# Performance work log

Measured on AMD Instinct MI355X. Metric: run time of the kernel, lower is better.

The kernel has to match this reference:

```python
import jax, jax.numpy as jnp
import numpy as np

HIDDEN = 1024
MOE_INTER = 512
SHARED_INTER = 2048
N_EXPERTS = 32
TOP_K = 6
N_GROUP = 8
TOPK_GROUP = 4
ROUTED_SCALE = 2.5


def setup_inputs() -> dict:
    key = jax.random.key(0)
    ks = jax.random.split(key, 6)
    s = 0.02
    return {
        "hidden_states": jax.random.normal(ks[0], (2, 1024, HIDDEN), jnp.float32),
        "gate_w": jax.random.normal(ks[1], (N_EXPERTS, HIDDEN), jnp.float32) * s,
        "e_bias": jnp.zeros((N_EXPERTS,), jnp.float32),  # e_score_correction_bias (non-trainable)
        "up_w": jax.random.normal(ks[2], (N_EXPERTS, MOE_INTER, HIDDEN), jnp.float32) * s,
        "down_w": jax.random.normal(ks[3], (N_EXPERTS, HIDDEN, MOE_INTER), jnp.float32) * s,
        "shared_up_w": jax.random.normal(ks[4], (SHARED_INTER, HIDDEN), jnp.float32) * s,
        "shared_down_w": jax.random.normal(ks[5], (HIDDEN, SHARED_INTER), jnp.float32) * s,
    }


def _relu2(x):
    # Nemotron-H 'relu2' activation: relu(x)^2
    return jnp.square(jax.nn.relu(x))


def _router(x, gate_w, e_bias):
    # x: [T, H] -> topk_idx [T, K] (int), topk_w [T, K] (fp32)
    T = x.shape[0]
    logits = x.astype(jnp.float32) @ gate_w.astype(jnp.float32).T  # [T, E]
    scores = jax.nn.sigmoid(logits)
    sc = scores + e_bias[None, :]
    # group-limited routing: top-2 sum per group, keep topk_group groups
    g = sc.reshape(T, N_GROUP, N_EXPERTS // N_GROUP)
    group_scores = jax.lax.top_k(g, 2)[0].sum(-1)                  # [T, G]
    group_idx = jax.lax.top_k(group_scores, TOPK_GROUP)[1]         # [T, TG]
    group_mask = jnp.zeros_like(group_scores).at[jnp.arange(T)[:, None], group_idx].set(1.0)
    score_mask = jnp.repeat(group_mask, N_EXPERTS // N_GROUP, axis=1)  # [T, E]
    masked = jnp.where(score_mask > 0, sc, 0.0)
    topk_idx = jax.lax.stop_gradient(jax.lax.top_k(masked, TOP_K)[1])  # torch path is @no_grad
    topk_w = jnp.take_along_axis(scores, topk_idx, axis=1)         # gather from unbiased scores
    topk_w = topk_w / (topk_w.sum(-1, keepdims=True) + 1e-20)      # norm_topk_prob
    topk_w = topk_w * ROUTED_SCALE
    return topk_idx, topk_w


def reference(hidden_states, gate_w, e_bias, up_w, down_w, shared_up_w, shared_down_w):
    B, S, H = hidden_states.shape
    x = hidden_states.reshape(-1, H)  # [T, H]
    T = x.shape[0]
    topk_idx, topk_w = _router(x, gate_w, e_bias)
    # combine weights as dense [T, E] (scatter of top-k weights)
    combine = jnp.zeros((T, N_EXPERTS), topk_w.dtype).at[jnp.arange(T)[:, None], topk_idx].add(topk_w)
    # dense-masked expert compute; weight applied on intermediate (equivalent since
    # down_proj is linear with no bias): out = sum_e w_te * down_e(act(up_e(x)))
    h = _relu2(jnp.einsum('th,eih->tei', x, up_w))   # [T, E, I]
    h = h * combine[:, :, None]
    moe_out = jnp.einsum('tei,ehi->th', h, down_w)   # [T, H]
    shared = _relu2(x @ shared_up_w.T) @ shared_down_w.T
    return (moe_out + shared).reshape(B, S, H)


if __name__ == "__main__":
    out = reference(**setup_inputs())
    print(out.shape, out.dtype)
```

## Files before the change

kernel.cpp:

```cpp
#include <hip/hip_runtime.h>

typedef unsigned short u16;
typedef __bf16 bf16x8 __attribute__((ext_vector_type(8)));
typedef float f32x4 __attribute__((ext_vector_type(4)));
typedef u16 u16x8 __attribute__((ext_vector_type(8)));

#define T_TOK 2048
#define HID   1024
#define NEXP  32
#define IM    512
#define SI    2048
#define TOPK  6
#define PLAN_MAX 160

__device__ __forceinline__ u16 f2bf(float f){
  unsigned u = __float_as_uint(f);
  u += 0x7FFFu + ((u >> 16) & 1u);
  return (u16)(u >> 16);
}

__device__ __forceinline__ void gll16(const void* g, void* l){
  __builtin_amdgcn_global_load_lds((const __attribute__((address_space(1))) void*)g,
                                   (__attribute__((address_space(3))) void*)l, 16, 0, 0);
}

__device__ __forceinline__ u16x8 cvt2(float4 a, float4 b){
  u16x8 o;
  o[0] = f2bf(a.x); o[1] = f2bf(a.y); o[2] = f2bf(a.z); o[3] = f2bf(a.w);
  o[4] = f2bf(b.x); o[5] = f2bf(b.y); o[6] = f2bf(b.z); o[7] = f2bf(b.w);
  return o;
}

__global__ __launch_bounds__(256) void prep_kernel(
    const float* __restrict__ x, const float4* __restrict__ upw, const float4* __restrict__ dnw,
    const float4* __restrict__ supw, const float4* __restrict__ sdnw,
    const float* __restrict__ gate, const float* __restrict__ ebias,
    u16x8* __restrict__ xb, u16x8* __restrict__ upb, u16x8* __restrict__ dnb,
    u16x8* __restrict__ supb, u16x8* __restrict__ sdnb,
    int* __restrict__ ce, float* __restrict__ cw, int* __restrict__ done){
  int blk = blockIdx.x;
  if (blk == 0 && threadIdx.x == 0) *done = 0;
  if (blk >= 512){
    const float4* s; u16x8* d; long i;
    if (blk < 16896){
      i = (long)(blk - 512) * 256 + threadIdx.x;
      if (i < 2097152L){ s = upw; d = upb; }
      else             { s = dnw; d = dnb; i -= 2097152L; }
    } else {
      i = (long)(blk - 16896) * 256 + threadIdx.x;
      if      (i < 262144L){ s = (const float4*)x; d = xb; }
      else if (i < 524288L){ s = supw; d = supb; i -= 262144L; }
      else                 { s = sdnw; d = sdnb; i -= 524288L; }
    }
    float4 a = s[2*i], b = s[2*i+1];
    d[i] = cvt2(a, b);
    return;
  }
  int wave = threadIdx.x >> 6;
  int lane = threadIdx.x & 63;
  int t = blk * 4 + wave;
  int e = lane & 31, half = lane >> 5;
  const float4* xv = (const float4*)(x + (size_t)t * HID);
  const float4* gv = (const float4*)(gate + (size_t)e * HID);
  double d0a = 0, d1a = 0, d2a = 0, d3a = 0;
  for (int i = half * 128; i < half * 128 + 128; i++){
    float4 a = xv[i], b = gv[i];
    d0a += (double)a.x * b.x; d1a += (double)a.y * b.y;
    d2a += (double)a.z * b.z; d3a += (double)a.w * b.w;
  }
  double acc = (d0a + d1a) + (d2a + d3a);
  acc += __shfl_xor(acc, 32);
  double score = 1.0 / (1.0 + exp(-acc));
  double sc = score + (double)ebias[e];
  double o1  = __shfl_xor(sc, 1);
  double hi  = fmax(sc, o1), lo = fmin(sc, o1);
  double ohi = __shfl_xor(hi, 2), olo = __shfl_xor(lo, 2);
  double gs  = (hi >= ohi) ? hi + fmax(lo, ohi) : ohi + fmax(olo, hi);
  int g = e >> 2;
  int rank = 0;
#pragma unroll
  for (int j = 0; j < 8; j++){
    double gj = __shfl(gs, j * 4);
    if (gj > gs || (gj == gs && j < g)) rank++;
  }
  double cur = (rank < 4) ? sc : 0.0;
  int sel_e[TOPK]; double sel_w[TOPK]; double wsum = 0.0;
#pragma unroll
  for (int k = 0; k < TOPK; k++){
    double bv = cur; int bi = lane;
#pragma unroll
    for (int m = 32; m >= 1; m >>= 1){
      double ov = __shfl_xor(bv, m); int oi = __shfl_xor(bi, m);
      if (ov > bv || (ov == bv && oi < bi)) { bv = ov; bi = oi; }
    }
    if ((bi & 31) == e) cur = -1e300;
    double ws = __shfl(score, bi);
    sel_e[k] = bi; sel_w[k] = ws; wsum += ws;
  }
  double scale = 2.5 / (wsum + 1e-20);
#pragma unroll
  for (int k = 0; k < TOPK; k++){
    if (lane == k){
      ce[t * TOPK + k] = sel_e[k] & 31;
      cw[t * TOPK + k] = (float)(sel_w[k] * scale);
    }
  }
}

__global__ __launch_bounds__(256) void build_plan_kernel(const int* __restrict__ ce,
                                                         const float* __restrict__ cw,
                                                         int* __restrict__ cnt,
                                                         int* __restrict__ tok,
                                                         float* __restrict__ wl,
                                                         int* __restrict__ done,
                                                         int* __restrict__ plan){
  int e = blockIdx.x;
  int tid = threadIdx.x, lane = tid & 63, wave = tid >> 6;
  __shared__ int wsum[4];
  __shared__ int lastflag;
  int running = 0;
  for (int base = 0; base < T_TOK * TOPK; base += 256){
    int i = base + tid;
    bool m = (ce[i] == e);
    unsigned long long bal = __ballot(m);
    int woff = __popcll(bal & ((1ull << lane) - 1ull));
    if (lane == 0) wsum[wave] = __popcll(bal);
    __syncthreads();
    int wbase = 0;
#pragma unroll
    for (int wv = 0; wv < 4; wv++) if (wv < wave) wbase += wsum[wv];
    int btot = wsum[0] + wsum[1] + wsum[2] + wsum[3];
    if (m){
      int t = i / TOPK, k = i - t * TOPK;
      int pos = running + wbase + woff;
      tok[e * T_TOK + pos] = (t << 3) | k;
      wl[e * T_TOK + pos] = cw[i];
    }
    running += btot;
    __syncthreads();
  }
  if (tid == 0){
    atomicExch(&cnt[e], running);
    __threadfence();
    lastflag = (atomicAdd(done, 1) == NEXP - 1);
  }
  __syncthreads();
  if (lastflag){
    __threadfence();
    if (tid < PLAN_MAX) plan[1 + tid] = -1;
    __syncthreads();
    if (tid == 0){
      int n = 0;
      for (int ee = 0; ee < NEXP; ee++){
        int c = (ee == e) ? running : cnt[ee];
        for (int tb = 0; tb < c; tb += 128) plan[1 + n++] = (tb << 8) | ee;
      }
      plan[0] = n;
    }
  }
}

__device__ __forceinline__ void gemm_pipe(
    const char* gA0, const char* gA1, const char* gB0, const char* gB1,
    u16* lA, u16* lB, int iters, int tid, int wrow, int wcol, int qsw, int l16,
    f32x4 acc[4][4])
{
  char* bA = (char*)lA + tid*16;
  char* bB = (char*)lB + tid*16;
#define STAGE(t, b) do { \
    gll16(gA0 + (size_t)(t)*64, bA + (b)*8192); \
    gll16(gA1 + (size_t)(t)*64, bA + (b)*8192 + 4096); \
    gll16(gB0 + (size_t)(t)*64, bB + (b)*8192); \
    gll16(gB1 + (size_t)(t)*64, bB + (b)*8192 + 4096); } while(0)
#define COMPUTE(rbuf) do { \
    const u16* rA = lA + (rbuf)*4096; \
    const u16* rB = lB + (rbuf)*4096; \
    bf16x8 af[4], bfr[4]; \
    _Pragma("unroll") \
    for (int mt = 0; mt < 4; mt++) af[mt]  = *(const bf16x8*)&rA[(wrow + mt*16 + l16)*32 + qsw*8]; \
    _Pragma("unroll") \
    for (int nt = 0; nt < 4; nt++) bfr[nt] = *(const bf16x8*)&rB[(wcol + nt*16 + l16)*32 + qsw*8]; \
    _Pragma("unroll") \
    for (int mt = 0; mt < 4; mt++) \
    _Pragma("unroll") \
      for (int nt = 0; nt < 4; nt++) \
        acc[mt][nt] = __builtin_amdgcn_mfma_f32_16x16x32_bf16(af[mt], bfr[nt], acc[mt][nt], 0, 0, 0); \
    } while(0)

  STAGE(0, 0); STAGE(1, 1);
  int rb = 0, sb = 2;
  for (int it = 0; it < iters - 2; ++it){
    STAGE(it + 2, sb);
    asm volatile("s_waitcnt vmcnt(8)" ::: "memory");
    __builtin_amdgcn_s_barrier();
    asm volatile("" ::: "memory");
    COMPUTE(rb);
    asm volatile("" ::: "memory");
    __builtin_amdgcn_s_barrier();
    asm volatile("" ::: "memory");
    rb = (rb + 1 == 3) ? 0 : rb + 1;
    sb = (sb + 1 == 3) ? 0 : sb + 1;
  }
  asm volatile("s_waitcnt vmcnt(4)" ::: "memory");
  __builtin_amdgcn_s_barrier();
  asm volatile("" ::: "memory");
  COMPUTE(rb);
  asm volatile("" ::: "memory");
  __builtin_amdgcn_s_barrier();
  asm volatile("" ::: "memory");
  rb = (rb + 1 == 3) ? 0 : rb + 1;
  asm volatile("s_waitcnt vmcnt(0)" ::: "memory");
  __builtin_amdgcn_s_barrier();
  asm volatile("" ::: "memory");
  COMPUTE(rb);
#undef STAGE
#undef COMPUTE
}

#define ACC_INIT f32x4 acc[4][4]; \
  _Pragma("unroll") for (int i_ = 0; i_ < 4; i_++) \
  _Pragma("unroll") for (int j_ = 0; j_ < 4; j_++) acc[i_][j_] = (f32x4){0.f,0.f,0.f,0.f};

#define GEO_INIT int tid = threadIdx.x; \
  int lane = tid & 63, wave = tid >> 6, quad = lane >> 4, l16 = lane & 15; \
  int wrow = (wave >> 1)*64, wcol = (wave & 1)*64; \
  int srow = tid >> 2; \
  int sseg = ((tid & 3) ^ ((tid >> 3) & 3)) * 16; \
  int qsw  = quad ^ ((l16 >> 1) & 3);

__global__ __launch_bounds__(256) void up_fused_kernel(
    const u16* __restrict__ xb, const u16* __restrict__ supb, const u16* __restrict__ upb,
    const int* __restrict__ cnt, const int* __restrict__ tok, const float* __restrict__ wl,
    const int* __restrict__ plan, u16* __restrict__ shh, u16* __restrict__ hws){
  __shared__ u16 lA[3*4096], lB[3*4096];
  GEO_INIT;
  int blk = blockIdx.x;
  if (blk < 256){
    int bm = (blk >> 4) * 128, bn = (blk & 15) * 128;
    const char* gA0 = (const char*)(xb + (size_t)(bm + srow)*HID) + sseg;
    const char* gA1 = (const char*)(xb + (size_t)(bm + 64 + srow)*HID) + sseg;
    const char* gB0 = (const char*)(supb + (size_t)(bn + srow)*HID) + sseg;
    const char* gB1 = (const char*)(supb + (size_t)(bn + 64 + srow)*HID) + sseg;
    ACC_INIT;
    gemm_pipe(gA0, gA1, gB0, gB1, lA, lB, HID/32, tid, wrow, wcol, qsw, l16, acc);
#pragma unroll
    for (int mt = 0; mt < 4; mt++)
#pragma unroll
      for (int nt = 0; nt < 4; nt++)
#pragma unroll
        for (int r = 0; r < 4; r++){
          int m = bm + wrow + mt*16 + quad*4 + r;
          int n = bn + wcol + nt*16 + l16;
          float v = acc[mt][nt][r]; v = fmaxf(v, 0.f); v *= v;
          shh[(size_t)m*SI + n] = f2bf(v);
        }
  } else {
    int eu = blk - 256;
    int pv = plan[1 + (eu >> 2)];
    if (pv < 0) return;
    int e = pv & 255;
    int tb = pv >> 8;
    int c = cnt[e];
    int bn = (eu & 3) * 128;
    const int* tl = tok + e * T_TOK;
    const float* wle = wl + e * T_TOK;
    int s0 = tb + srow;      if (s0 > c-1) s0 = c-1;
    int s1 = tb + 64 + srow; if (s1 > c-1) s1 = c-1;
    int t0 = tl[s0] >> 3, t1 = tl[s1] >> 3;
    const char* gA0 = (const char*)(xb + (size_t)t0*HID) + sseg;
    const char* gA1 = (const char*)(xb + (size_t)t1*HID) + sseg;
    const u16* Bb = upb + (size_t)e * IM * HID;
    const char* gB0 = (const char*)(Bb + (size_t)(bn + srow)*HID) + sseg;
    const char* gB1 = (const char*)(Bb + (size_t)(bn + 64 + srow)*HID) + sseg;
    ACC_INIT;
    gemm_pipe(gA0, gA1, gB0, gB1, lA, lB, HID/32, tid, wrow, wcol, qsw, l16, acc);
#pragma unroll
    for (int mt = 0; mt < 4; mt++)
#pragma unroll
      for (int r = 0; r < 4; r++){
        int s = tb + wrow + mt*16 + quad*4 + r;
        if (s < c){
          int code = tl[s];
          float w = wle[s];
          size_t hb = ((size_t)(code >> 3) * TOPK + (code & 7)) * IM;
#pragma unroll
          for (int nt = 0; nt < 4; nt++){
            float v = acc[mt][nt][r]; v = fmaxf(v, 0.f); v = v * v * w;
            hws[hb + bn + wcol + nt*16 + l16] = f2bf(v);
          }
        }
      }
  }
}

__global__ __launch_bounds__(256) void down_fused_kernel(
    const u16* __restrict__ shh, const u16* __restrict__ sdnb,
    const u16* __restrict__ hws, const u16* __restrict__ dnb,
    const int* __restrict__ cnt, const int* __restrict__ tok, const int* __restrict__ plan,
    float* __restrict__ out){
  __shared__ u16 lA[3*4096], lB[3*4096];
  GEO_INIT;
  int blk = blockIdx.x;
  if (blk < 128){
    int bm = (blk >> 3)*128, bn = (blk & 7)*128;
    const char* gA0 = (const char*)(shh + (size_t)(bm + srow)*SI) + sseg;
    const char* gA1 = (const char*)(shh + (size_t)(bm + 64 + srow)*SI) + sseg;
    const char* gB0 = (const char*)(sdnb + (size_t)(bn + srow)*SI) + sseg;
    const char* gB1 = (const char*)(sdnb + (size_t)(bn + 64 + srow)*SI) + sseg;
    ACC_INIT;
    gemm_pipe(gA0, gA1, gB0, gB1, lA, lB, SI/32, tid, wrow, wcol, qsw, l16, acc);
#pragma unroll
    for (int mt = 0; mt < 4; mt++)
#pragma unroll
      for (int nt = 0; nt < 4; nt++)
#pragma unroll
        for (int r = 0; r < 4; r++){
          int m = bm + wrow + mt*16 + quad*4 + r;
          int n = bn + wcol + nt*16 + l16;
          unsafeAtomicAdd(&out[(size_t)m*HID + n], acc[mt][nt][r]);
        }
  } else {
    int eu = blk - 128;
    int pv = plan[1 + (eu >> 3)];
    if (pv < 0) return;
    int e = pv & 255;
    int tb = pv >> 8;
    int c = cnt[e];
    int bn = (eu & 7) * 128;
    const int* tl = tok + e * T_TOK;
    int s0 = tb + srow;      if (s0 > c-1) s0 = c-1;
    int s1 = tb + 64 + srow; if (s1 > c-1) s1 = c-1;
    int c0 = tl[s0], c1 = tl[s1];
    const char* gA0 = (const char*)(hws + ((size_t)(c0 >> 3)*TOPK + (c0 & 7))*IM) + sseg;
    const char* gA1 = (const char*)(hws + ((size_t)(c1 >> 3)*TOPK + (c1 & 7))*IM) + sseg;
    const u16* Bb = dnb + (size_t)e * HID * IM;
    const char* gB0 = (const char*)(Bb + (size_t)(bn + srow)*IM) + sseg;
    const char* gB1 = (const char*)(Bb + (size_t)(bn + 64 + srow)*IM) + sseg;
    ACC_INIT;
    gemm_pipe(gA0, gA1, gB0, gB1, lA, lB, IM/32, tid, wrow, wcol, qsw, l16, acc);
#pragma unroll
    for (int mt = 0; mt < 4; mt++)
#pragma unroll
      for (int r = 0; r < 4; r++){
        int s = tb + wrow + mt*16 + quad*4 + r;
        if (s < c){
          int code = tl[s];
          float* ob = out + (size_t)(code >> 3) * HID;
#pragma unroll
          for (int nt = 0; nt < 4; nt++)
            unsafeAtomicAdd(&ob[bn + wcol + nt*16 + l16], acc[mt][nt][r]);
        }
      }
  }
}

extern "C" void kernel_launch(void* const* d_in, const int* in_sizes, int n_in,
                              void* d_out, int out_size, void* d_ws, size_t ws_size,
                              hipStream_t stream) {
  const float* x    = (const float*)d_in[0];
  const float* gate = (const float*)d_in[1];
  const float* eb   = (const float*)d_in[2];
  const float* upw  = (const float*)d_in[3];
  const float* dnw  = (const float*)d_in[4];
  const float* supw = (const float*)d_in[5];
  const float* sdnw = (const float*)d_in[6];
  float* out = (float*)d_out;

  char* w = (char*)d_ws;
  size_t o = 0;
  int*   cnt  = (int*)(w + o);   o += 1024;
  int*   plan = (int*)(w + o);   o += 1024;
  int*   ce   = (int*)(w + o);   o += (size_t)T_TOK * TOPK * 4;
  float* cw   = (float*)(w + o); o += (size_t)T_TOK * TOPK * 4;
  int*   tok  = (int*)(w + o);   o += (size_t)NEXP * T_TOK * 4;
  float* wl   = (float*)(w + o); o += (size_t)NEXP * T_TOK * 4;
  u16*   xb   = (u16*)(w + o);   o += (size_t)T_TOK * HID * 2;
  u16*   dnb  = (u16*)(w + o);   o += (size_t)NEXP * HID * IM * 2;
  u16*   hws  = (u16*)(w + o);   o += (size_t)T_TOK * TOPK * IM * 2;
  u16*   upb  = (u16*)(w + o);   o += (size_t)NEXP * IM * HID * 2;
  u16*   supb = (u16*)(w + o);   o += (size_t)SI * HID * 2;
  u16*   sdnb = (u16*)(w + o);   o += (size_t)HID * SI * 2;
  u16*   shh  = (u16*)(w + o);   o += (size_t)T_TOK * SI * 2;
  int*   done = cnt + 32;

  hipMemsetAsync(out, 0, (size_t)T_TOK * HID * 4, stream);
  prep_kernel<<<19968, 256, 0, stream>>>(
      x, (const float4*)upw, (const float4*)dnw, (const float4*)supw, (const float4*)sdnw,
      gate, eb, (u16x8*)xb, (u16x8*)upb, (u16x8*)dnb, (u16x8*)supb, (u16x8*)sdnb,
      ce, cw, done);
  build_plan_kernel<<<NEXP, 256, 0, stream>>>(ce, cw, cnt, tok, wl, done, plan);
  up_fused_kernel<<<896, 256, 0, stream>>>(xb, supb, upb, cnt, tok, wl, plan, shh, hws);
  down_fused_kernel<<<1408, 256, 0, stream>>>(shh, sdnb, hws, dnb, cnt, tok, plan, out);
}
```

Before: 335.7 us.

## Widen conversion to 16 floats per thread with nontemporal loads; swizzle GEMM block order

The fp32-to-bf16 weight conversion in the prep kernel now handles 16 floats per thread using nontemporal loads, which halves the grid size and keeps streamed weights from polluting cache. The up and down GEMM kernels remap blockIdx with a stride-8 interleave so that neighbouring blocks spread across XCDs, which changes how L2 is shared. The remap could hurt L2 locality if neighbouring tiles were previously reusing data on the same XCD.

```diff
diff --git a/kernel.cpp b/kernel.cpp
--- a/kernel.cpp
+++ b/kernel.cpp
@@ -24,16 +24,20 @@
                                    (__attribute__((address_space(3))) void*)l, 16, 0, 0);
 }
 
-__device__ __forceinline__ u16x8 cvt2(float4 a, float4 b){
+__device__ __forceinline__ f32x4 ntld(const f32x4* p){
+  return __builtin_nontemporal_load(p);
+}
+
+__device__ __forceinline__ u16x8 cvt2(f32x4 a, f32x4 b){
   u16x8 o;
-  o[0] = f2bf(a.x); o[1] = f2bf(a.y); o[2] = f2bf(a.z); o[3] = f2bf(a.w);
-  o[4] = f2bf(b.x); o[5] = f2bf(b.y); o[6] = f2bf(b.z); o[7] = f2bf(b.w);
+  o[0] = f2bf(a[0]); o[1] = f2bf(a[1]); o[2] = f2bf(a[2]); o[3] = f2bf(a[3]);
+  o[4] = f2bf(b[0]); o[5] = f2bf(b[1]); o[6] = f2bf(b[2]); o[7] = f2bf(b[3]);
   return o;
 }
 
 __global__ __launch_bounds__(256) void prep_kernel(
-    const float* __restrict__ x, const float4* __restrict__ upw, const float4* __restrict__ dnw,
-    const float4* __restrict__ supw, const float4* __restrict__ sdnw,
+    const float* __restrict__ x, const float* __restrict__ upw, const float* __restrict__ dnw,
+    const float* __restrict__ supw, const float* __restrict__ sdnw,
     const float* __restrict__ gate, const float* __restrict__ ebias,
     u16x8* __restrict__ xb, u16x8* __restrict__ upb, u16x8* __restrict__ dnb,
     u16x8* __restrict__ supb, u16x8* __restrict__ sdnb,
@@ -41,19 +45,17 @@
   int blk = blockIdx.x;
   if (blk == 0 && threadIdx.x == 0) *done = 0;
   if (blk >= 512){
-    const float4* s; u16x8* d; long i;
-    if (blk < 16896){
-      i = (long)(blk - 512) * 256 + threadIdx.x;
-      if (i < 2097152L){ s = upw; d = upb; }
-      else             { s = dnw; d = dnb; i -= 2097152L; }
-    } else {
-      i = (long)(blk - 16896) * 256 + threadIdx.x;
-      if      (i < 262144L){ s = (const float4*)x; d = xb; }
-      else if (i < 524288L){ s = supw; d = supb; i -= 262144L; }
-      else                 { s = sdnw; d = sdnb; i -= 524288L; }
-    }
-    float4 a = s[2*i], b = s[2*i+1];
-    d[i] = cvt2(a, b);
+    long i = (long)(blk - 512) * 256 + threadIdx.x;
+    const f32x4* s; u16x8* d;
+    if      (i <  131072L){ s = (const f32x4*)x;    d = xb;   }
+    else if (i < 1179648L){ s = (const f32x4*)upw;  d = upb;  i -=  131072L; }
+    else if (i < 2228224L){ s = (const f32x4*)dnw;  d = dnb;  i -= 1179648L; }
+    else if (i < 2359296L){ s = (const f32x4*)supw; d = supb; i -= 2228224L; }
+    else                  { s = (const f32x4*)sdnw; d = sdnb; i -= 2359296L; }
+    f32x4 a0 = ntld(s + 4*i), a1 = ntld(s + 4*i + 1);
+    f32x4 a2 = ntld(s + 4*i + 2), a3 = ntld(s + 4*i + 3);
+    d[2*i]     = cvt2(a0, a1);
+    d[2*i + 1] = cvt2(a2, a3);
     return;
   }
   int wave = threadIdx.x >> 6;
@@ -168,10 +170,10 @@
   char* bA = (char*)lA + tid*16;
   char* bB = (char*)lB + tid*16;
 #define STAGE(t, b) do { \
-    gll16(gA0 + (size_t)(t)*64, bA + (b)*8192); \
-    gll16(gA1 + (size_t)(t)*64, bA + (b)*8192 + 4096); \
-    gll16(gB0 + (size_t)(t)*64, bB + (b)*8192); \
-    gll16(gB1 + (size_t)(t)*64, bB + (b)*8192 + 4096); } while(0)
+    gll16(gA0 + (size_t)(t)*64, bA + (size_t)(b)*8192); \
+    gll16(gA1 + (size_t)(t)*64, bA + (size_t)(b)*8192 + 4096); \
+    gll16(gB0 + (size_t)(t)*64, bB + (size_t)(b)*8192); \
+    gll16(gB1 + (size_t)(t)*64, bB + (size_t)(b)*8192 + 4096); } while(0)
 #define COMPUTE(rbuf) do { \
     const u16* rA = lA + (rbuf)*4096; \
     const u16* rB = lB + (rbuf)*4096; \
@@ -234,7 +236,8 @@
     const int* __restrict__ plan, u16* __restrict__ shh, u16* __restrict__ hws){
   __shared__ u16 lA[3*4096], lB[3*4096];
   GEO_INIT;
-  int blk = blockIdx.x;
+  int h = blockIdx.x;
+  int blk = (h % 112) * 8 + h / 112;
   if (blk < 256){
     int bm = (blk >> 4) * 128, bn = (blk & 15) * 128;
     const char* gA0 = (const char*)(xb + (size_t)(bm + srow)*HID) + sseg;
@@ -300,7 +303,8 @@
     float* __restrict__ out){
   __shared__ u16 lA[3*4096], lB[3*4096];
   GEO_INIT;
-  int blk = blockIdx.x;
+  int h = blockIdx.x;
+  int blk = (h % 176) * 8 + h / 176;
   if (blk < 128){
     int bm = (blk >> 3)*128, bn = (blk & 7)*128;
     const char* gA0 = (const char*)(shh + (size_t)(bm + srow)*SI) + sseg;
@@ -383,10 +387,10 @@
   u16*   shh  = (u16*)(w + o);   o += (size_t)T_TOK * SI * 2;
   int*   done = cnt + 32;
 
-  hipMemsetAsync(out, 0, (size_t)T_TOK * HID * 4, stream);
-  prep_kernel<<<19968, 256, 0, stream>>>(
-      x, (const float4*)upw, (const float4*)dnw, (const float4*)supw, (const float4*)sdnw,
-      gate, eb, (u16x8*)xb, (u16x8*)upb, (u16x8*)dnb, (u16x8*)supb, (u16x8*)sdnb,
+  (void)hipMemsetAsync(out, 0, (size_t)T_TOK * HID * 4, stream);
+  prep_kernel<<<10240, 256, 0, stream>>>(
+      x, upw, dnw, supw, sdnw, gate, eb,
+      (u16x8*)xb, (u16x8*)upb, (u16x8*)dnb, (u16x8*)supb, (u16x8*)sdnb,
       ce, cw, done);
   build_plan_kernel<<<NEXP, 256, 0, stream>>>(ce, cw, cnt, tok, wl, done, plan);
   up_fused_kernel<<<896, 256, 0, stream>>>(xb, supb, upb, cnt, tok, wl, plan, shh, hws);
```

After: 389.2 us. +16.0%, slower.
